# Kernel optimization log

Hardware: AMD Instinct MI355X
Metric: run time of the kernel (lower is better)

Reference implementation:

```python
import jax, jax.numpy as jnp
import numpy as np

N_HEADS = 16

def setup_inputs() -> dict:
    key = jax.random.key(0)
    k1, k2, k3 = jax.random.split(key, 3)
    B, T, C = 4, 2048, 1024
    x = jax.random.normal(k1, (B, T, C), dtype=jnp.float32)
    W_kqv = jax.random.normal(k2, (C, 3 * C), dtype=jnp.float32) * (C ** -0.5)
    W_proj = jax.random.normal(k3, (C, C), dtype=jnp.float32) * (C ** -0.5)
    return {"x": x, "W_kqv": W_kqv, "W_proj": W_proj}


def reference(x, W_kqv, W_proj):
    # x: (B,T,C). Dropout layers are identity in eval mode (p treated as 0).
    B, T, C = x.shape
    H = N_HEADS
    D = C // H
    dk = D ** -0.5
    kqv = x @ W_kqv                     # (B,T,3C)
    kqv = kqv.reshape(B, T, 3, H, D).transpose(2, 0, 3, 1, 4)  # (3,B,H,T,D)
    k, q, v = kqv[0], kqv[1], kqv[2]    # note: k first, matching source
    scores = jnp.einsum('bhqd,bhkd->bhqk', q, k) * dk  # (B,H,T,T)
    attn = jax.nn.softmax(scores, axis=-1)
    out = jnp.einsum('bhqk,bhkd->bhqd', attn, v)       # (B,H,T,D)
    out = out.transpose(0, 2, 1, 3).reshape(B, T, C)   # (B,T,C)
    return out @ W_proj
```

## Files before the change

### kernel.cpp

```cpp
#include <hip/hip_runtime.h>
#include <hip/hip_bf16.h>

typedef unsigned short ushort_t;
typedef __attribute__((ext_vector_type(8))) short short8;
typedef __attribute__((ext_vector_type(4))) float f32x4;

__device__ __forceinline__ ushort_t f2bf(float f) {
    union { float f; unsigned int u; } v; v.f = f;
    unsigned int r = v.u + 0x7fffu + ((v.u >> 16) & 1u);
    return (ushort_t)(r >> 16);
}

__device__ __forceinline__ unsigned int cvtpk(float lo, float hi) {
    unsigned int r;
    asm("v_cvt_pk_bf16_f32 %0, %1, %2" : "=v"(r) : "v"(lo), "v"(hi));
    return r;
}

__device__ __forceinline__ void async16(const ushort_t* g, ushort_t* l) {
    __builtin_amdgcn_global_load_lds((const __attribute__((address_space(1))) void*)g,
                                     (__attribute__((address_space(3))) void*)l,
                                     16, 0, 0);
}

__global__ void cvt_bf16(const float* __restrict__ src, ushort_t* __restrict__ dst) {
    int i = (blockIdx.x * 256 + threadIdx.x) * 8;
    float4 f0 = *(const float4*)(src + i);
    float4 f1 = *(const float4*)(src + i + 4);
    union { uint4 v; ushort_t e[8]; } d;
    d.e[0]=f2bf(f0.x); d.e[1]=f2bf(f0.y); d.e[2]=f2bf(f0.z); d.e[3]=f2bf(f0.w);
    d.e[4]=f2bf(f1.x); d.e[5]=f2bf(f1.y); d.e[6]=f2bf(f1.z); d.e[7]=f2bf(f1.w);
    *(uint4*)(dst + i) = d.v;
}

__global__ void transpose_w(const float* __restrict__ src, ushort_t* __restrict__ dst,
                            int R, int C, int lo, int hi, float scale) {
    __shared__ ushort_t tile[32][33];
    const int bx = blockIdx.x * 32, by = blockIdx.y * 32;
    const int tx = threadIdx.x, ty = threadIdx.y;
    const float s = (bx + tx >= lo && bx + tx < hi) ? scale : 1.0f;
    #pragma unroll
    for (int i = 0; i < 32; i += 8)
        tile[ty + i][tx] = f2bf(src[(size_t)(by + ty + i) * C + bx + tx] * s);
    __syncthreads();
    #pragma unroll
    for (int i = 0; i < 32; i += 8)
        dst[(size_t)(bx + ty + i) * R + by + tx] = tile[tx][ty + i];
}

template <bool CF32, bool VOUT>
__global__ __launch_bounds__(256, 2)
void gemm_bt(const ushort_t* __restrict__ A, const ushort_t* __restrict__ Bt,
             void* __restrict__ Cv, ushort_t* __restrict__ vT, int M, int N, int K) {
    constexpr int BK = 32;
    __shared__ ushort_t As[128 * BK];
    __shared__ ushort_t Bs[128 * BK];

    const int tid  = threadIdx.x;
    const int wave = tid >> 6;
    const int lane = tid & 63;
    const int quad = lane >> 4;
    const int l16  = lane & 15;
    const int m0 = blockIdx.x * 128;
    const int n0 = blockIdx.y * 128;
    const int wm = (wave >> 1) * 64;
    const int wn = (wave & 1) * 64;
    const int rA = (lane >> 2);
    const int cA = (lane & 3) * 8;

    f32x4 acc[4][4] = {};

    for (int k0 = 0; k0 < K; k0 += BK) {
        __syncthreads();
        #pragma unroll
        for (int u = 0; u < 2; ++u) {
            int c = wave * 2 + u;
            int row = c * 16 + rA;
            async16(A  + (size_t)(m0 + row) * K + k0 + cA, As + c * 512);
            async16(Bt + (size_t)(n0 + row) * K + k0 + cA, Bs + c * 512);
        }
        __syncthreads();

        short8 af[4], bf[4];
        #pragma unroll
        for (int mt = 0; mt < 4; ++mt)
            af[mt] = *(const short8*)(As + (wm + mt * 16 + l16) * BK + quad * 8);
        #pragma unroll
        for (int nt = 0; nt < 4; ++nt)
            bf[nt] = *(const short8*)(Bs + (wn + nt * 16 + l16) * BK + quad * 8);

        #pragma unroll
        for (int mt = 0; mt < 4; ++mt)
            #pragma unroll
            for (int nt = 0; nt < 4; ++nt)
                acc[mt][nt] = __builtin_amdgcn_mfma_f32_16x16x32_bf16(
                    af[mt], bf[nt], acc[mt][nt], 0, 0, 0);
    }

    if constexpr (VOUT) {
        if (n0 >= 2048) {
            const int b  = m0 >> 11;
            const int tb = m0 & 2047;
            const int h0 = (n0 - 2048) >> 6;
            ushort_t* tileT = As;
            __syncthreads();
            #pragma unroll
            for (int hh = 0; hh < 2; ++hh) {
                if ((wave & 1) == hh) {
                    #pragma unroll
                    for (int nt = 0; nt < 4; ++nt) {
                        int d = nt * 16 + l16;
                        #pragma unroll
                        for (int mt = 0; mt < 4; ++mt) {
                            int t = wm + mt * 16 + quad * 4;
                            uint2 w;
                            w.x = cvtpk(acc[mt][nt][0], acc[mt][nt][1]);
                            w.y = cvtpk(acc[mt][nt][2], acc[mt][nt][3]);
                            *(uint2*)(tileT + d * 128 + t) = w;
                        }
                    }
                }
                __syncthreads();
                #pragma unroll
                for (int i = 0; i < 4; ++i) {
                    int c = i * 256 + tid;
                    int d = c >> 4, cp = (c & 15) * 8;
                    *(uint4*)(vT + ((size_t)((b * 16 + h0 + hh) * 64 + d)) * 2048 + tb + cp) =
                        *(const uint4*)(tileT + d * 128 + cp);
                }
                __syncthreads();
            }
            return;
        }
    }

    #pragma unroll
    for (int mt = 0; mt < 4; ++mt) {
        #pragma unroll
        for (int r = 0; r < 4; ++r) {
            int row = m0 + wm + mt * 16 + quad * 4 + r;
            if constexpr (CF32) {
                float* op = (float*)Cv + (size_t)row * N + n0 + wn + l16;
                #pragma unroll
                for (int nt = 0; nt < 4; ++nt) op[nt * 16] = acc[mt][nt][r];
            } else {
                ushort_t* op = (ushort_t*)Cv + (size_t)row * N + n0 + wn + l16;
                #pragma unroll
                for (int nt = 0; nt < 4; ++nt) op[nt * 16] = f2bf(acc[mt][nt][r]);
            }
        }
    }
}

__global__ __launch_bounds__(256, 3)
void attn_kernel(const ushort_t* __restrict__ kqv, const ushort_t* __restrict__ vT,
                 ushort_t* __restrict__ aout) {
    constexpr int T = 2048;
    constexpr int NT = T / 64;

    __shared__ __align__(16) ushort_t smem[24576];
    ushort_t* const Ps = smem + 16384;

    const int tid  = threadIdx.x;
    const int wave = tid >> 6;
    const int lane = tid & 63;
    const int quad = lane >> 4;
    const int l16  = lane & 15;

    const int lin = blockIdx.x;
    const int qt  = (lin >> 3) & 15;
    const int bh  = ((lin >> 7) << 3) | (lin & 7);
    const int b   = bh >> 4, h = bh & 15;
    const int q0  = qt * 128;
    const size_t rowBase = (size_t)b * T;

    short8 qf[2][2];
    #pragma unroll
    for (int mt = 0; mt < 2; ++mt) {
        const ushort_t* qp = kqv + (rowBase + q0 + wave * 32 + mt * 16 + l16) * 3072 + 1024 + h * 64;
        qf[mt][0] = *(const short8*)(qp + quad * 8);
        qf[mt][1] = *(const short8*)(qp + 32 + quad * 8);
    }

    const ushort_t* kbase = kqv + rowBase * 3072 + h * 64;
    const ushort_t* vbase = vT + (size_t)bh * 64 * 2048;
    ushort_t* const pw = Ps + wave * 2048;

    const int swz = l16 & 7;
    const int qh  = quad >> 1;
    int wrow[2], gxo[4];
    #pragma unroll
    for (int mt = 0; mt < 2; ++mt) wrow[mt] = (mt * 16 + l16) * 64 + (quad & 1) * 4;
    #pragma unroll
    for (int nt = 0; nt < 4; ++nt) gxo[nt] = ((nt * 2 + qh) ^ swz) * 8;

    auto stage = [&](ushort_t* dk, ushort_t* dv, int kk) {
        #pragma unroll
        for (int u = 0; u < 2; ++u) {
            int g = u * 256 + tid;
            int row = g >> 3, pos = g & 7;
            int c = pos ^ (row & 7);
            async16(kbase + (size_t)(kk + row) * 3072 + c * 8, dk + g * 8);
            async16(vbase + (size_t)row * 2048 + kk + c * 8, dv + g * 8);
        }
    };

    f32x4 O[2][4] = {};
    float lrow[2] = {};

    stage(smem, smem + 4096, 0);

    #pragma unroll 2
    for (int t = 0; t < NT; ++t) {
        ushort_t* const Ks = smem + ((t & 1) << 13);
        ushort_t* const Vs = Ks + 4096;
        ushort_t* const Kn = smem + (((t & 1) ^ 1) << 13);

        __builtin_amdgcn_s_barrier();
        if (t + 1 < NT) {
            stage(Kn, Kn + 4096, (t + 1) * 64);
            asm volatile("s_waitcnt vmcnt(4)" ::: "memory");
        } else {
            asm volatile("s_waitcnt vmcnt(0)" ::: "memory");
        }
        __builtin_amdgcn_s_barrier();
        __builtin_amdgcn_sched_barrier(0);

        f32x4 S[2][4];
        #pragma unroll
        for (int nt = 0; nt < 4; ++nt) {
            int key = nt * 16 + l16;
            const ushort_t* kr = Ks + key * 64;
            short8 kf0 = *(const short8*)(kr + ((quad     ^ (l16 & 7)) * 8));
            short8 kf1 = *(const short8*)(kr + (((quad+4) ^ (l16 & 7)) * 8));
            #pragma unroll
            for (int mt = 0; mt < 2; ++mt) {
                f32x4 s = {0.f, 0.f, 0.f, 0.f};
                s = __builtin_amdgcn_mfma_f32_16x16x32_bf16(kf0, qf[mt][0], s, 0, 0, 0);
                s = __builtin_amdgcn_mfma_f32_16x16x32_bf16(kf1, qf[mt][1], s, 0, 0, 0);
                S[mt][nt] = s;
            }
        }

        #pragma unroll
        for (int mt = 0; mt < 2; ++mt) {
            #pragma unroll
            for (int nt = 0; nt < 4; ++nt) {
                float p0 = __builtin_amdgcn_exp2f(S[mt][nt][0]);
                float p1 = __builtin_amdgcn_exp2f(S[mt][nt][1]);
                float p2 = __builtin_amdgcn_exp2f(S[mt][nt][2]);
                float p3 = __builtin_amdgcn_exp2f(S[mt][nt][3]);
                lrow[mt] += (p0 + p1) + (p2 + p3);
                uint2 w;
                w.x = cvtpk(p0, p1);
                w.y = cvtpk(p2, p3);
                *(uint2*)(pw + wrow[mt] + gxo[nt]) = w;
            }
        }
        asm volatile("s_waitcnt lgkmcnt(0)" ::: "memory");

        short8 pf[2][2];
        #pragma unroll
        for (int mt = 0; mt < 2; ++mt)
            #pragma unroll
            for (int f = 0; f < 2; ++f)
                pf[mt][f] = *(const short8*)(pw + (mt * 16 + l16) * 64 + (((f * 4 + quad) ^ swz) * 8));

        #pragma unroll
        for (int dt = 0; dt < 4; ++dt) {
            int d = dt * 16 + l16;
            const ushort_t* vr = Vs + d * 64;
            short8 vf0 = *(const short8*)(vr + ((quad     ^ (l16 & 7)) * 8));
            short8 vf1 = *(const short8*)(vr + (((quad+4) ^ (l16 & 7)) * 8));
            #pragma unroll
            for (int mt = 0; mt < 2; ++mt) {
                O[mt][dt] = __builtin_amdgcn_mfma_f32_16x16x32_bf16(pf[mt][0], vf0, O[mt][dt], 0, 0, 0);
                O[mt][dt] = __builtin_amdgcn_mfma_f32_16x16x32_bf16(pf[mt][1], vf1, O[mt][dt], 0, 0, 0);
            }
        }
    }

    #pragma unroll
    for (int mt = 0; mt < 2; ++mt) {
        float s = lrow[mt];
        s += __shfl_xor(s, 16, 64);
        s += __shfl_xor(s, 32, 64);
        float inv[4];
        #pragma unroll
        for (int r = 0; r < 4; ++r)
            inv[r] = 1.f / __shfl(s, quad * 4 + r, 64);
        #pragma unroll
        for (int dt = 0; dt < 4; ++dt)
            #pragma unroll
            for (int r = 0; r < 4; ++r) {
                int row = q0 + wave * 32 + mt * 16 + quad * 4 + r;
                aout[(rowBase + row) * 1024 + h * 64 + dt * 16 + l16] = f2bf(O[mt][dt][r] * inv[r]);
            }
    }
}

extern "C" void kernel_launch(void* const* d_in, const int* in_sizes, int n_in,
                              void* d_out, int out_size, void* d_ws, size_t ws_size,
                              hipStream_t stream) {
    const float* x     = (const float*)d_in[0];
    const float* Wkqv  = (const float*)d_in[1];
    const float* Wproj = (const float*)d_in[2];
    float* out = (float*)d_out;

    constexpr int M = 8192, K = 1024;
    constexpr float SC = 0.18033688011112042f;
    char* ws = (char*)d_ws;
    ushort_t* kqv    = (ushort_t*)(ws);
    ushort_t* vT     = (ushort_t*)(ws + 50331648);
    ushort_t* xb     = (ushort_t*)(ws + 67108864);
    ushort_t* aout   = xb;
    ushort_t* WkqvT  = (ushort_t*)(ws + 83886080);
    ushort_t* WprojT = (ushort_t*)(ws + 90177536);

    cvt_bf16<<<4096, 256, 0, stream>>>(x, xb);
    transpose_w<<<dim3(96, 32), dim3(32, 8), 0, stream>>>(Wkqv, WkqvT, 1024, 3072, 1024, 2048, SC);
    transpose_w<<<dim3(32, 32), dim3(32, 8), 0, stream>>>(Wproj, WprojT, 1024, 1024, 0, 0, 1.0f);

    gemm_bt<false, true><<<dim3(M / 128, 3072 / 128), 256, 0, stream>>>(xb, WkqvT, kqv, vT, M, 3072, K);
    attn_kernel<<<1024, 256, 0, stream>>>(kqv, vT, aout);
    gemm_bt<true, false><<<dim3(M / 128, 1024 / 128), 256, 0, stream>>>(aout, WprojT, out, nullptr, M, 1024, K);
}
```

Before: 266.1 us.

## Double-buffer LDS tiles in bf16 GEMM to overlap global loads with MFMA

Makes the As/Bs shared tiles double-buffered and issues the async global-to-LDS load for the next K-tile before computing on the current one. Partial vmcnt waits and raw s_barrier calls replace the two full __syncthreads per iteration, so load latency can hide behind the MFMA work. This doubles LDS use per block, which could affect the 2-blocks-per-CU occupancy, and depends on the vmcnt count matching the outstanding loads.

```diff
diff --git a/kernel.cpp b/kernel.cpp
--- a/kernel.cpp
+++ b/kernel.cpp
@@ -53,8 +53,8 @@
 void gemm_bt(const ushort_t* __restrict__ A, const ushort_t* __restrict__ Bt,
              void* __restrict__ Cv, ushort_t* __restrict__ vT, int M, int N, int K) {
     constexpr int BK = 32;
-    __shared__ ushort_t As[128 * BK];
-    __shared__ ushort_t Bs[128 * BK];
+    __shared__ ushort_t As[2][128 * BK];
+    __shared__ ushort_t Bs[2][128 * BK];
 
     const int tid  = threadIdx.x;
     const int wave = tid >> 6;
@@ -68,26 +68,40 @@
     const int rA = (lane >> 2);
     const int cA = (lane & 3) * 8;
 
-    f32x4 acc[4][4] = {};
-
-    for (int k0 = 0; k0 < K; k0 += BK) {
-        __syncthreads();
+    auto stage = [&](int buf, int k0) {
         #pragma unroll
         for (int u = 0; u < 2; ++u) {
             int c = wave * 2 + u;
             int row = c * 16 + rA;
-            async16(A  + (size_t)(m0 + row) * K + k0 + cA, As + c * 512);
-            async16(Bt + (size_t)(n0 + row) * K + k0 + cA, Bs + c * 512);
-        }
-        __syncthreads();
+            async16(A  + (size_t)(m0 + row) * K + k0 + cA, As[buf] + c * 512);
+            async16(Bt + (size_t)(n0 + row) * K + k0 + cA, Bs[buf] + c * 512);
+        }
+    };
+
+    f32x4 acc[4][4] = {};
+    const int NT = K / BK;
+    stage(0, 0);
+
+    #pragma unroll 2
+    for (int t = 0; t < NT; ++t) {
+        const int cur = t & 1;
+        __builtin_amdgcn_s_barrier();
+        if (t + 1 < NT) {
+            stage(cur ^ 1, (t + 1) * BK);
+            asm volatile("s_waitcnt vmcnt(4)" ::: "memory");
+        } else {
+            asm volatile("s_waitcnt vmcnt(0)" ::: "memory");
+        }
+        __builtin_amdgcn_s_barrier();
+        __builtin_amdgcn_sched_barrier(0);
 
         short8 af[4], bf[4];
         #pragma unroll
         for (int mt = 0; mt < 4; ++mt)
-            af[mt] = *(const short8*)(As + (wm + mt * 16 + l16) * BK + quad * 8);
+            af[mt] = *(const short8*)(As[cur] + (wm + mt * 16 + l16) * BK + quad * 8);
         #pragma unroll
         for (int nt = 0; nt < 4; ++nt)
-            bf[nt] = *(const short8*)(Bs + (wn + nt * 16 + l16) * BK + quad * 8);
+            bf[nt] = *(const short8*)(Bs[cur] + (wn + nt * 16 + l16) * BK + quad * 8);
 
         #pragma unroll
         for (int mt = 0; mt < 4; ++mt)
@@ -102,7 +116,7 @@
             const int b  = m0 >> 11;
             const int tb = m0 & 2047;
             const int h0 = (n0 - 2048) >> 6;
-            ushort_t* tileT = As;
+            ushort_t* tileT = &As[0][0];
             __syncthreads();
             #pragma unroll
             for (int hh = 0; hh < 2; ++hh) {
```

Result: no change. 269.4 us (+1.3%).

## Halve per-wave P scratch in LDS to raise attention and GEMM occupancy

Applied to the files above, without the earlier changes.

The attention kernel now round-trips P through LDS one 16-row tile at a time, so each wave's scratch region shrinks from 2048 to 1024 elements and total shared memory drops from 48KB to 40KB. This allows the launch bound to rise from 3 to 4 blocks per CU, and the GEMM launch bound also rises from 2 to 3. V fragments are preloaded into registers before the P write/read loop. The trade-off is extra waitcnt serialization per mt tile, and tighter register budgets from the higher launch bounds, which may cause spills.

```diff
diff --git a/kernel.cpp b/kernel.cpp
--- a/kernel.cpp
+++ b/kernel.cpp
@@ -49,7 +49,7 @@
 }
 
 template <bool CF32, bool VOUT>
-__global__ __launch_bounds__(256, 2)
+__global__ __launch_bounds__(256, 3)
 void gemm_bt(const ushort_t* __restrict__ A, const ushort_t* __restrict__ Bt,
              void* __restrict__ Cv, ushort_t* __restrict__ vT, int M, int N, int K) {
     constexpr int BK = 32;
@@ -152,13 +152,13 @@
     }
 }
 
-__global__ __launch_bounds__(256, 3)
+__global__ __launch_bounds__(256, 4)
 void attn_kernel(const ushort_t* __restrict__ kqv, const ushort_t* __restrict__ vT,
                  ushort_t* __restrict__ aout) {
     constexpr int T = 2048;
     constexpr int NT = T / 64;
 
-    __shared__ __align__(16) ushort_t smem[24576];
+    __shared__ __align__(16) ushort_t smem[20480];
     ushort_t* const Ps = smem + 16384;
 
     const int tid  = threadIdx.x;
@@ -184,13 +184,12 @@
 
     const ushort_t* kbase = kqv + rowBase * 3072 + h * 64;
     const ushort_t* vbase = vT + (size_t)bh * 64 * 2048;
-    ushort_t* const pw = Ps + wave * 2048;
+    ushort_t* const pw = Ps + wave * 1024;
 
     const int swz = l16 & 7;
     const int qh  = quad >> 1;
-    int wrow[2], gxo[4];
-    #pragma unroll
-    for (int mt = 0; mt < 2; ++mt) wrow[mt] = (mt * 16 + l16) * 64 + (quad & 1) * 4;
+    const int wrow = l16 * 64 + (quad & 1) * 4;
+    int gxo[4];
     #pragma unroll
     for (int nt = 0; nt < 4; ++nt) gxo[nt] = ((nt * 2 + qh) ^ swz) * 8;
 
@@ -242,6 +241,7 @@
             }
         }
 
+        uint2 w[2][4];
         #pragma unroll
         for (int mt = 0; mt < 2; ++mt) {
             #pragma unroll
@@ -251,31 +251,32 @@
                 float p2 = __builtin_amdgcn_exp2f(S[mt][nt][2]);
                 float p3 = __builtin_amdgcn_exp2f(S[mt][nt][3]);
                 lrow[mt] += (p0 + p1) + (p2 + p3);
-                uint2 w;
-                w.x = cvtpk(p0, p1);
-                w.y = cvtpk(p2, p3);
-                *(uint2*)(pw + wrow[mt] + gxo[nt]) = w;
-            }
-        }
-        asm volatile("s_waitcnt lgkmcnt(0)" ::: "memory");
-
-        short8 pf[2][2];
-        #pragma unroll
-        for (int mt = 0; mt < 2; ++mt)
-            #pragma unroll
-            for (int f = 0; f < 2; ++f)
-                pf[mt][f] = *(const short8*)(pw + (mt * 16 + l16) * 64 + (((f * 4 + quad) ^ swz) * 8));
-
+                w[mt][nt].x = cvtpk(p0, p1);
+                w[mt][nt].y = cvtpk(p2, p3);
+            }
+        }
+
+        short8 vf[4][2];
         #pragma unroll
         for (int dt = 0; dt < 4; ++dt) {
-            int d = dt * 16 + l16;
-            const ushort_t* vr = Vs + d * 64;
-            short8 vf0 = *(const short8*)(vr + ((quad     ^ (l16 & 7)) * 8));
-            short8 vf1 = *(const short8*)(vr + (((quad+4) ^ (l16 & 7)) * 8));
-            #pragma unroll
-            for (int mt = 0; mt < 2; ++mt) {
-                O[mt][dt] = __builtin_amdgcn_mfma_f32_16x16x32_bf16(pf[mt][0], vf0, O[mt][dt], 0, 0, 0);
-                O[mt][dt] = __builtin_amdgcn_mfma_f32_16x16x32_bf16(pf[mt][1], vf1, O[mt][dt], 0, 0, 0);
+            const ushort_t* vr = Vs + (dt * 16 + l16) * 64;
+            vf[dt][0] = *(const short8*)(vr + ((quad     ^ (l16 & 7)) * 8));
+            vf[dt][1] = *(const short8*)(vr + (((quad+4) ^ (l16 & 7)) * 8));
+        }
+
+        #pragma unroll
+        for (int mt = 0; mt < 2; ++mt) {
+            #pragma unroll
+            for (int nt = 0; nt < 4; ++nt)
+                *(uint2*)(pw + wrow + gxo[nt]) = w[mt][nt];
+            asm volatile("s_waitcnt lgkmcnt(0)" ::: "memory");
+            short8 pf0 = *(const short8*)(pw + l16 * 64 + ((quad       ^ swz) * 8));
+            short8 pf1 = *(const short8*)(pw + l16 * 64 + (((4 + quad) ^ swz) * 8));
+            asm volatile("s_waitcnt lgkmcnt(0)" ::: "memory");
+            #pragma unroll
+            for (int dt = 0; dt < 4; ++dt) {
+                O[mt][dt] = __builtin_amdgcn_mfma_f32_16x16x32_bf16(pf0, vf[dt][0], O[mt][dt], 0, 0, 0);
+                O[mt][dt] = __builtin_amdgcn_mfma_f32_16x16x32_bf16(pf1, vf[dt][1], O[mt][dt], 0, 0, 0);
             }
         }
     }
```

New measurement: 333.3 us. 25.3% more time.
